# Kernel optimization log

Measured on AMD Instinct MI355X. Metric: run time of the kernel, lower is better.

The kernel has to match this reference:

```python
import jax, jax.numpy as jnp
import numpy as np
from jax import lax

VOCAB, EMB, HID, TAGS = 50000, 300, 512, 50
T, B = 256, 64
H = HID // 2  # per-direction LSTM hidden


def _lstm(xs, W_ih, W_hh, b_ih, b_hh):
    # xs: [T, B, E]; PyTorch gate order i, f, g, o
    xp = jnp.einsum('tbe,ge->tbg', xs, W_ih) + b_ih  # precompute input projection

    def step(carry, x_t):
        h, c = carry
        gates = x_t + h @ W_hh.T + b_hh
        i, f, g, o = jnp.split(gates, 4, axis=-1)
        c = jax.nn.sigmoid(f) * c + jax.nn.sigmoid(i) * jnp.tanh(g)
        h = jax.nn.sigmoid(o) * jnp.tanh(c)
        return (h, c), h

    h0 = jnp.zeros((xs.shape[1], H), xs.dtype)
    _, hs = lax.scan(step, (h0, h0), xp)
    return hs  # [T, B, H]


def setup_inputs() -> dict:
    key = jax.random.key(0)
    ks = jax.random.split(key, 16)
    s_emb = 1.0
    s_lstm = 1.0 / np.sqrt(H)
    inp = {
        'x': jax.random.randint(ks[0], (T, B), 0, VOCAB),
        'y': jax.random.randint(ks[1], (T, B), 0, TAGS),
        'mask': jnp.ones((T, B), dtype=bool),
        'emb': jax.random.normal(ks[2], (VOCAB, EMB), jnp.float32) * s_emb,
        'W_ih_f': jax.random.uniform(ks[3], (4 * H, EMB), jnp.float32, -s_lstm, s_lstm),
        'W_hh_f': jax.random.uniform(ks[4], (4 * H, H), jnp.float32, -s_lstm, s_lstm),
        'b_ih_f': jax.random.uniform(ks[5], (4 * H,), jnp.float32, -s_lstm, s_lstm),
        'b_hh_f': jax.random.uniform(ks[6], (4 * H,), jnp.float32, -s_lstm, s_lstm),
        'W_ih_b': jax.random.uniform(ks[7], (4 * H, EMB), jnp.float32, -s_lstm, s_lstm),
        'W_hh_b': jax.random.uniform(ks[8], (4 * H, H), jnp.float32, -s_lstm, s_lstm),
        'b_ih_b': jax.random.uniform(ks[9], (4 * H,), jnp.float32, -s_lstm, s_lstm),
        'b_hh_b': jax.random.uniform(ks[10], (4 * H,), jnp.float32, -s_lstm, s_lstm),
        'W_out': jax.random.normal(ks[11], (TAGS, HID), jnp.float32) * 0.02,
        'b_out': jnp.zeros((TAGS,), jnp.float32),
        'start_trans': jax.random.uniform(ks[12], (TAGS,), jnp.float32, -0.1, 0.1),
        'end_trans': jax.random.uniform(ks[13], (TAGS,), jnp.float32, -0.1, 0.1),
        'trans': jax.random.uniform(ks[14], (TAGS, TAGS), jnp.float32, -0.1, 0.1),
    }
    return inp


def _emissions(x, emb, W_ih_f, W_hh_f, b_ih_f, b_hh_f, W_ih_b, W_hh_b, b_ih_b, b_hh_b, W_out, b_out):
    e = emb[x]                                   # [T, B, EMB]
    h_f = _lstm(e, W_ih_f, W_hh_f, b_ih_f, b_hh_f)
    h_b = _lstm(e[::-1], W_ih_b, W_hh_b, b_ih_b, b_hh_b)[::-1]
    h = jnp.concatenate([h_f, h_b], axis=-1)    # [T, B, HID]; dropout in eval mode = identity
    return jnp.einsum('tbh,kh->tbk', h, W_out) + b_out  # [T, B, TAGS]


def _crf_loss(em, y, mask, start_trans, end_trans, trans):
    maskf = mask.astype(em.dtype)
    tt = jnp.arange(1, T)
    bb = jnp.arange(B)
    # numerator: score of the gold path (torchcrf _compute_score)
    num = start_trans[y[0]] + em[0, bb, y[0]]
    num = num + (trans[y[:-1], y[1:]] * maskf[1:]).sum(0)
    num = num + (em[tt[:, None], bb[None, :], y[1:]] * maskf[1:]).sum(0)
    last_idx = mask.astype(jnp.int32).sum(0) - 1
    num = num + end_trans[y[last_idx, bb]]
    # denominator: forward algorithm (log-sum-exp DP)
    def fstep(score, inp):
        em_t, m_t = inp
        nxt = jax.nn.logsumexp(score[:, :, None] + trans[None] + em_t[:, None, :], axis=1)
        return jnp.where(m_t[:, None], nxt, score), None
    score0 = start_trans[None] + em[0]          # [B, TAGS]
    score, _ = lax.scan(fstep, score0, (em[1:], mask[1:]))
    denom = jax.nn.logsumexp(score + end_trans[None], axis=-1)
    return -(num - denom).sum()                 # loss = -llh (sum reduction)


def _crf_decode(em, mask, start_trans, end_trans, trans):
    def vstep(score, inp):
        em_t, m_t = inp
        combo = score[:, :, None] + trans[None]  # [B, prev, cur]
        idx = combo.argmax(1)
        nxt = combo.max(1) + em_t
        return jnp.where(m_t[:, None], nxt, score), idx
    score0 = start_trans[None] + em[0]
    score, history = lax.scan(vstep, score0, (em[1:], mask[1:]))  # history: [T-1, B, TAGS]
    last = jnp.argmax(score + end_trans[None], axis=-1)           # [B]
    def bstep(cur, inp):
        hist_t, m_t = inp
        prev = jnp.take_along_axis(hist_t, cur[:, None], axis=1)[:, 0]
        return jnp.where(m_t, prev, cur), cur
    tag0, rest = lax.scan(bstep, last, (history, mask[1:]), reverse=True)
    return jnp.concatenate([tag0[None], rest], axis=0)            # [T, B] int


def reference(x, y, mask, emb, W_ih_f, W_hh_f, b_ih_f, b_hh_f, W_ih_b, W_hh_b, b_ih_b, b_hh_b, W_out, b_out, start_trans, end_trans, trans):
    em = _emissions(x, emb, W_ih_f, W_hh_f, b_ih_f, b_hh_f, W_ih_b, W_hh_b, b_ih_b, b_hh_b, W_out, b_out)
    loss = _crf_loss(em, y, mask, start_trans, end_trans, trans)
    pred = _crf_decode(em, mask, start_trans, end_trans, trans)
    return (loss, pred)
```

## Files before the change

kernel.cpp:

```cpp
#include <hip/hip_runtime.h>
#include <math.h>

#define T_LEN 256
#define BATCH 64
#define NEMB  300
#define NHID  256
#define NG4   1024
#define NTAGS 50

typedef float    f32x4 __attribute__((ext_vector_type(4)));

static constexpr size_t XP_OFF  = 0;
static constexpr size_t XP_SZ   = (size_t)2 * 1024 * 16384;
static constexpr size_t HC_OFF  = XP_OFF + XP_SZ;
static constexpr size_t HC_SZ   = (size_t)T_LEN * 512 * 64;
static constexpr size_t HX_OFF  = HC_OFF + HC_SZ;
static constexpr size_t HX_SZ   = (size_t)2 * 2 * 256 * 64;
static constexpr size_t EM_OFF  = HX_OFF + HX_SZ;
static constexpr size_t EM_SZ   = (size_t)T_LEN * BATCH * NTAGS;
static constexpr size_t LLH_OFF = EM_OFF + EM_SZ;
static constexpr size_t CNT_OFF = LLH_OFF + 64;

__global__ __launch_bounds__(256)
void k_init(float* __restrict__ ws) {
    unsigned int* f = (unsigned int*)(ws + CNT_OFF);
    int i = blockIdx.x * 256 + threadIdx.x;
    if (i < 512) f[i] = 0u;
}

__global__ __launch_bounds__(256)
void k_xp(const int* __restrict__ x, const float* __restrict__ emb,
          const float* __restrict__ Wf, const float* __restrict__ Wb,
          const float* __restrict__ bihf, const float* __restrict__ bhhf,
          const float* __restrict__ bihb, const float* __restrict__ bhhb,
          float* __restrict__ xpT) {
    __shared__ float As[8 * 136];
    __shared__ float Ws[8 * 136];
    __shared__ int   xrow[128];

    const int tid  = threadIdx.x;
    const int row0 = blockIdx.x * 128;
    const int col0 = blockIdx.y * 128;
    const int dir  = col0 >> 10;
    const int g0   = col0 & 1023;
    const float* __restrict__ W   = dir ? Wb   : Wf;
    const float* __restrict__ bih = dir ? bihb : bihf;
    const float* __restrict__ bhh = dir ? bhhb : bhhf;

    if (tid < 128) xrow[tid] = x[row0 + tid];
    __syncthreads();

    float acc[8][8];
#pragma unroll
    for (int i = 0; i < 8; i++)
#pragma unroll
        for (int j = 0; j < 8; j++) acc[i][j] = 0.f;

    const int ty = tid >> 4;
    const int tx = tid & 15;

    for (int kc = 0; kc < NEMB; kc += 8) {
#pragma unroll
        for (int q = 0; q < 4; q++) {
            int idx = tid + 256 * q;
            int r   = idx >> 3;
            int kk  = idx & 7;
            int k   = kc + kk;
            float av = 0.f, wv = 0.f;
            if (k < NEMB) {
                av = emb[(size_t)xrow[r] * NEMB + k];
                wv = W[(size_t)(g0 + r) * NEMB + k];
            }
            As[kk * 136 + r] = av;
            Ws[kk * 136 + r] = wv;
        }
        __syncthreads();
#pragma unroll
        for (int kk = 0; kk < 8; kk++) {
            float4 a0 = *(const float4*)&As[kk * 136 + 8 * ty];
            float4 a1 = *(const float4*)&As[kk * 136 + 8 * ty + 4];
            float4 b0 = *(const float4*)&Ws[kk * 136 + 8 * tx];
            float4 b1 = *(const float4*)&Ws[kk * 136 + 8 * tx + 4];
            float a[8] = {a0.x,a0.y,a0.z,a0.w,a1.x,a1.y,a1.z,a1.w};
            float w[8] = {b0.x,b0.y,b0.z,b0.w,b1.x,b1.y,b1.z,b1.w};
#pragma unroll
            for (int i = 0; i < 8; i++)
#pragma unroll
                for (int j = 0; j < 8; j++) acc[i][j] += a[i] * w[j];
        }
        __syncthreads();
    }

#pragma unroll
    for (int jj = 0; jj < 8; jj++) {
        const int c = g0 + 8 * tx + jj;
        const float bb = bih[c] + bhh[c];
        float4 v0 = make_float4(acc[0][jj] + bb, acc[1][jj] + bb,
                                acc[2][jj] + bb, acc[3][jj] + bb);
        float4 v1 = make_float4(acc[4][jj] + bb, acc[5][jj] + bb,
                                acc[6][jj] + bb, acc[7][jj] + bb);
        float* dst = xpT + ((size_t)dir * 1024 + c) * 16384 + row0 + 8 * ty;
        *(float4*)dst       = v0;
        *(float4*)(dst + 4) = v1;
    }
}

__global__ __launch_bounds__(256, 1)
void k_lstm(const float* __restrict__ xpT, const float* __restrict__ Whf,
            const float* __restrict__ Whb, float* __restrict__ hcatT,
            float* __restrict__ hx, unsigned int* __restrict__ cnt) {
    __shared__ float hs[BATCH * NHID];
    __shared__ float accS[8 * BATCH];

    const int wg    = blockIdx.x;
    const int dir   = wg >> 7;
    const int wslot = wg & 127;
    const int j0    = wslot * 2;
    const int tid   = threadIdx.x;
    const int w     = tid >> 6;
    const int lane  = tid & 63;
    const int rg    = w & 1;
    const int bhalf = w >> 1;
    const int kthr  = lane >> 3;
    const int bthr  = lane & 7;
    const int jme   = j0 + rg;

    const float* __restrict__ Wh  = dir ? Whb : Whf;
    const float* __restrict__ xpd = xpT + (size_t)dir * 1024 * 16384;
    float* __restrict__ hxd = hx + (size_t)dir * 32768;
    unsigned int* __restrict__ cntd = cnt + dir * 256;

    float wreg[4][32];
#pragma unroll
    for (int g = 0; g < 4; ++g) {
        const float4* src = (const float4*)(Wh + ((size_t)(g * 256 + jme)) * 256 + kthr * 32);
#pragma unroll
        for (int q = 0; q < 8; ++q) {
            float4 v = src[q];
            wreg[g][q * 4 + 0] = v.x;
            wreg[g][q * 4 + 1] = v.y;
            wreg[g][q * 4 + 2] = v.z;
            wreg[g][q * 4 + 3] = v.w;
        }
    }
    float creg[2] = {0.f, 0.f};

    for (int s = 0; s < T_LEN; ++s) {
        const int t = dir ? (T_LEN - 1 - s) : s;

        float xq[2][4];
        if (w == 0) {
#pragma unroll
            for (int jj = 0; jj < 2; ++jj)
#pragma unroll
                for (int g = 0; g < 4; ++g)
                    xq[jj][g] = xpd[((size_t)(g * 256 + j0 + jj)) * 16384 + t * 64 + lane];
        }

        float acc[4][4];
#pragma unroll
        for (int g = 0; g < 4; ++g)
#pragma unroll
            for (int bi = 0; bi < 4; ++bi) acc[g][bi] = 0.f;

        if (s > 0) {
            if (tid == 0) {
                while (__hip_atomic_load(&cntd[s - 1], __ATOMIC_RELAXED,
                                         __HIP_MEMORY_SCOPE_AGENT) < 128u) {
                    __builtin_amdgcn_s_sleep(4);
                }
            }
            __syncthreads();

            const float* hsrc = hxd + (size_t)((s - 1) & 1) * 16384;
            f32x4 stv[16];
#pragma unroll
            for (int q = 0; q < 16; ++q) {
                const float* ap = hsrc + q * 1024 + tid * 4;
                asm volatile("global_load_dwordx4 %0, %1, off sc0 sc1"
                             : "=v"(stv[q]) : "v"(ap));
            }
            const int b0   = (tid & 15) * 4;
            const int rot4 = 4 * (tid & 7);
            asm volatile("s_waitcnt vmcnt(8)" ::: "memory");
#pragma unroll
            for (int q = 0; q < 8; ++q) {
                const int kk = q * 16 + (tid >> 4);
                const int sw = (kk & ~31) | ((kk + rot4) & 31);
                hs[(b0 + 0) * 256 + sw] = stv[q].x;
                hs[(b0 + 1) * 256 + sw] = stv[q].y;
                hs[(b0 + 2) * 256 + sw] = stv[q].z;
                hs[(b0 + 3) * 256 + sw] = stv[q].w;
            }
            asm volatile("s_waitcnt vmcnt(0)" ::: "memory");
#pragma unroll
            for (int q = 8; q < 16; ++q) {
                const int kk = q * 16 + (tid >> 4);
                const int sw = (kk & ~31) | ((kk + rot4) & 31);
                hs[(b0 + 0) * 256 + sw] = stv[q].x;
                hs[(b0 + 1) * 256 + sw] = stv[q].y;
                hs[(b0 + 2) * 256 + sw] = stv[q].z;
                hs[(b0 + 3) * 256 + sw] = stv[q].w;
            }
            __syncthreads();

#pragma unroll
            for (int bi = 0; bi < 4; ++bi) {
                const int b = bhalf * 32 + bthr * 4 + bi;
                const float* hb = &hs[b * 256 + kthr * 32];
                const int rot = bthr;
#pragma unroll
                for (int c8 = 0; c8 < 8; ++c8) {
                    const float4 h4 = *(const float4*)&hb[4 * ((c8 + rot) & 7)];
#pragma unroll
                    for (int g = 0; g < 4; ++g) {
                        acc[g][bi] += h4.x * wreg[g][4 * c8 + 0]
                                    + h4.y * wreg[g][4 * c8 + 1]
                                    + h4.z * wreg[g][4 * c8 + 2]
                                    + h4.w * wreg[g][4 * c8 + 3];
                    }
                }
            }
#pragma unroll
            for (int g = 0; g < 4; ++g)
#pragma unroll
                for (int bi = 0; bi < 4; ++bi) {
                    float v = acc[g][bi];
                    v += __shfl_xor(v, 8);
                    v += __shfl_xor(v, 16);
                    v += __shfl_xor(v, 32);
                    acc[g][bi] = v;
                }
            if (kthr == 0) {
#pragma unroll
                for (int g = 0; g < 4; ++g) {
                    float4 v = make_float4(acc[g][0], acc[g][1], acc[g][2], acc[g][3]);
                    *(float4*)&accS[(rg * 4 + g) * 64 + bhalf * 32 + bthr * 4] = v;
                }
            }
            __syncthreads();
        }

        if (w == 0) {
#pragma unroll
            for (int jj = 0; jj < 2; ++jj) {
                float gi = xq[jj][0], gf = xq[jj][1], gg = xq[jj][2], go = xq[jj][3];
                if (s > 0) {
                    gi += accS[(jj * 4 + 0) * 64 + lane];
                    gf += accS[(jj * 4 + 1) * 64 + lane];
                    gg += accS[(jj * 4 + 2) * 64 + lane];
                    go += accS[(jj * 4 + 3) * 64 + lane];
                }
                float ig = 1.f / (1.f + expf(-gi));
                float fg = 1.f / (1.f + expf(-gf));
                float tg = tanhf(gg);
                float og = 1.f / (1.f + expf(-go));
                float cn = fg * creg[jj] + ig * tg;
                creg[jj] = cn;
                float hv = og * tanhf(cn);
                hcatT[(size_t)t * 32768 + (size_t)(dir * 256 + j0 + jj) * 64 + lane] = hv;
                float* hp = &hxd[(size_t)(s & 1) * 16384 + (j0 + jj) * 64 + lane];
                asm volatile("global_store_dword %0, %1, off sc0 sc1"
                             :: "v"(hp), "v"(hv) : "memory");
            }
            if (s < T_LEN - 1) {
                asm volatile("s_waitcnt vmcnt(0)" ::: "memory");
                if (lane == 0) {
                    __hip_atomic_fetch_add(&cntd[s], 1u, __ATOMIC_RELAXED,
                                           __HIP_MEMORY_SCOPE_AGENT);
                }
            }
        }
    }
}

__global__ __launch_bounds__(256)
void k_em(const float* __restrict__ hcatT, const float* __restrict__ Wout,
          const float* __restrict__ bout, float* __restrict__ em) {
    __shared__ float Ws[52 * 132];
    __shared__ float ht[128 * 64];
    const int t   = blockIdx.x;
    const int tid = threadIdx.x;
    const int b   = tid & 63;
    const int tg  = tid >> 6;
    const int tagbase = tg * 13;

    float acc[13];
#pragma unroll
    for (int i = 0; i < 13; i++) acc[i] = 0.f;

    for (int k0 = 0; k0 < 512; k0 += 128) {
        __syncthreads();
#pragma unroll
        for (int q = 0; q < 25; q++) {
            int idx = tid + 256 * q;
            if (idx < 6400) {
                int tag = idx >> 7, kk = idx & 127;
                Ws[tag * 132 + kk] = Wout[(size_t)tag * 512 + k0 + kk];
            }
        }
#pragma unroll
        for (int q = 0; q < 32; q++) {
            int idx = tid + 256 * q;
            ht[idx] = hcatT[(size_t)t * 32768 + (size_t)k0 * 64 + idx];
        }
        __syncthreads();
        for (int kk = 0; kk < 128; kk++) {
            float hv = ht[kk * 64 + b];
#pragma unroll
            for (int i = 0; i < 13; i++)
                acc[i] += hv * Ws[(tagbase + i) * 132 + kk];
        }
    }
#pragma unroll
    for (int i = 0; i < 13; i++) {
        int tag = tagbase + i;
        if (tag < NTAGS)
            em[((size_t)t * BATCH + b) * NTAGS + tag] = acc[i] + bout[tag];
    }
}

__global__ __launch_bounds__(64)
void k_crf_loss(const float* __restrict__ em, const int* __restrict__ y,
                const float* __restrict__ st, const float* __restrict__ et,
                const float* __restrict__ tr, float* __restrict__ llh) {
    __shared__ float trs[2500];
    __shared__ float score[NTAGS];
    __shared__ float red[64];
    const int b   = blockIdx.x;
    const int tid = threadIdx.x;

#pragma unroll
    for (int q = 0; q < 40; q++) {
        int idx = tid + 64 * q;
        if (idx < 2500) trs[idx] = tr[idx];
    }
    __syncthreads();

    float part = 0.f;
    for (int t = tid; t < T_LEN; t += 64) {
        int yt = y[t * BATCH + b];
        if (t == 0) {
            part += st[yt] + em[(size_t)b * NTAGS + yt];
        } else {
            int yp = y[(t - 1) * BATCH + b];
            part += trs[yp * NTAGS + yt] + em[((size_t)t * BATCH + b) * NTAGS + yt];
        }
    }
    red[tid] = part;
    __syncthreads();
    for (int off = 32; off > 0; off >>= 1) {
        if (tid < off) red[tid] += red[tid + off];
        __syncthreads();
    }

    if (tid < NTAGS) score[tid] = st[tid] + em[(size_t)b * NTAGS + tid];
    __syncthreads();

    for (int t = 1; t < T_LEN; t++) {
        float ns = 0.f;
        if (tid < NTAGS) {
            float m = -1e30f;
            for (int p = 0; p < NTAGS; p++) {
                float v = score[p] + trs[p * NTAGS + tid];
                m = fmaxf(m, v);
            }
            float ssum = 0.f;
            for (int p = 0; p < NTAGS; p++) {
                float v = score[p] + trs[p * NTAGS + tid];
                ssum += expf(v - m);
            }
            ns = m + logf(ssum) + em[((size_t)t * BATCH + b) * NTAGS + tid];
        }
        __syncthreads();
        if (tid < NTAGS) score[tid] = ns;
        __syncthreads();
    }

    if (tid == 0) {
        float m = -1e30f;
        for (int cc = 0; cc < NTAGS; cc++) m = fmaxf(m, score[cc] + et[cc]);
        float ssum = 0.f;
        for (int cc = 0; cc < NTAGS; cc++) ssum += expf(score[cc] + et[cc] - m);
        float denom = m + logf(ssum);
        float num = red[0] + et[y[(T_LEN - 1) * BATCH + b]];
        llh[b] = num - denom;
    }
}

__global__ __launch_bounds__(64)
void k_viterbi(const float* __restrict__ em, const float* __restrict__ st,
               const float* __restrict__ et, const float* __restrict__ tr,
               float* __restrict__ out) {
    __shared__ float trs[2500];
    __shared__ float score[NTAGS];
    __shared__ unsigned char hist[(T_LEN - 1) * NTAGS];
    const int b   = blockIdx.x;
    const int tid = threadIdx.x;

#pragma unroll
    for (int q = 0; q < 40; q++) {
        int idx = tid + 64 * q;
        if (idx < 2500) trs[idx] = tr[idx];
    }
    if (tid < NTAGS) score[tid] = st[tid] + em[(size_t)b * NTAGS + tid];
    __syncthreads();

    for (int t = 1; t < T_LEN; t++) {
        float ns = 0.f;
        int am = 0;
        if (tid < NTAGS) {
            float m = -1e30f;
            for (int p = 0; p < NTAGS; p++) {
                float v = score[p] + trs[p * NTAGS + tid];
                if (v > m) { m = v; am = p; }
            }
            ns = m + em[((size_t)t * BATCH + b) * NTAGS + tid];
        }
        __syncthreads();
        if (tid < NTAGS) {
            score[tid] = ns;
            hist[(t - 1) * NTAGS + tid] = (unsigned char)am;
        }
        __syncthreads();
    }

    if (tid == 0) {
        float m = -1e30f;
        int cur = 0;
        for (int cc = 0; cc < NTAGS; cc++) {
            float v = score[cc] + et[cc];
            if (v > m) { m = v; cur = cc; }
        }
        out[1 + (T_LEN - 1) * BATCH + b] = (float)cur;
        for (int t = T_LEN - 2; t >= 0; t--) {
            cur = hist[t * NTAGS + cur];
            out[1 + t * BATCH + b] = (float)cur;
        }
    }
}

__global__ __launch_bounds__(64)
void k_loss_final(const float* __restrict__ llh, float* __restrict__ out) {
    __shared__ float red[64];
    const int tid = threadIdx.x;
    red[tid] = llh[tid];
    __syncthreads();
    for (int off = 32; off > 0; off >>= 1) {
        if (tid < off) red[tid] += red[tid + off];
        __syncthreads();
    }
    if (tid == 0) out[0] = -red[0];
}

extern "C" void kernel_launch(void* const* d_in, const int* in_sizes, int n_in,
                              void* d_out, int out_size, void* d_ws, size_t ws_size,
                              hipStream_t stream) {
    const int*   x    = (const int*)d_in[0];
    const int*   y    = (const int*)d_in[1];
    const float* emb  = (const float*)d_in[3];
    const float* Wihf = (const float*)d_in[4];
    const float* Whhf = (const float*)d_in[5];
    const float* bihf = (const float*)d_in[6];
    const float* bhhf = (const float*)d_in[7];
    const float* Wihb = (const float*)d_in[8];
    const float* Whhb = (const float*)d_in[9];
    const float* bihb = (const float*)d_in[10];
    const float* bhhb = (const float*)d_in[11];
    const float* Wout = (const float*)d_in[12];
    const float* bout = (const float*)d_in[13];
    const float* st   = (const float*)d_in[14];
    const float* et   = (const float*)d_in[15];
    const float* tr   = (const float*)d_in[16];

    float* out  = (float*)d_out;
    float* ws   = (float*)d_ws;
    float* xpT  = ws + XP_OFF;
    float* hcatT= ws + HC_OFF;
    float* hx   = ws + HX_OFF;
    float* em   = ws + EM_OFF;
    float* llh  = ws + LLH_OFF;
    unsigned int* cnt = (unsigned int*)(ws + CNT_OFF);

    hipLaunchKernelGGL(k_init, dim3(2), dim3(256), 0, stream, ws);

    dim3 g1(128, 16);
    hipLaunchKernelGGL(k_xp, g1, dim3(256), 0, stream,
                       x, emb, Wihf, Wihb, bihf, bhhf, bihb, bhhb, xpT);

    hipLaunchKernelGGL(k_lstm, dim3(256), dim3(256), 0, stream,
                       xpT, Whhf, Whhb, hcatT, hx, cnt);

    hipLaunchKernelGGL(k_em, dim3(T_LEN), dim3(256), 0, stream, hcatT, Wout, bout, em);

    hipLaunchKernelGGL(k_crf_loss, dim3(BATCH), dim3(64), 0, stream, em, y, st, et, tr, llh);

    hipLaunchKernelGGL(k_viterbi, dim3(BATCH), dim3(64), 0, stream, em, st, et, tr, out);

    hipLaunchKernelGGL(k_loss_final, dim3(1), dim3(64), 0, stream, llh, out);
}
```

Before: 3.475 ms.

## Shard LSTM step barrier counters across cache lines and stagger h loads

Replaces the single per-step arrival counter with eight counters, one per group of 16 workgroups, each padded onto its own 64-byte stride. A full wavefront now polls all eight with a ballot and a shorter sleep, which is meant to cut atomic contention and shorten barrier latency on the grid-wide recurrence. Each workgroup also rotates the order of its hidden-state loads by its slot index, to spread simultaneous reads across memory channels. The launch adds about 30 KB of dynamic shared memory, apparently to force one workgroup per CU. In exchange, the init kernel has to clear a much larger counter array, and every wait does more polling traffic.

Result: slower. 4.330 ms (+24.6%).

```diff
diff --git a/kernel.cpp b/kernel.cpp
--- a/kernel.cpp
+++ b/kernel.cpp
@@ -20,12 +20,13 @@
 static constexpr size_t EM_SZ   = (size_t)T_LEN * BATCH * NTAGS;
 static constexpr size_t LLH_OFF = EM_OFF + EM_SZ;
 static constexpr size_t CNT_OFF = LLH_OFF + 64;
+static constexpr int    CNT_DWORDS = 2 * 256 * 128;
 
 __global__ __launch_bounds__(256)
 void k_init(float* __restrict__ ws) {
     unsigned int* f = (unsigned int*)(ws + CNT_OFF);
     int i = blockIdx.x * 256 + threadIdx.x;
-    if (i < 512) f[i] = 0u;
+    if (i < CNT_DWORDS) f[i] = 0u;
 }
 
 __global__ __launch_bounds__(256)
@@ -111,6 +112,7 @@
             float* __restrict__ hx, unsigned int* __restrict__ cnt) {
     __shared__ float hs[BATCH * NHID];
     __shared__ float accS[8 * BATCH];
+    extern __shared__ float dynpad[];
 
     const int wg    = blockIdx.x;
     const int dir   = wg >> 7;
@@ -125,10 +127,13 @@
     const int bthr  = lane & 7;
     const int jme   = j0 + rg;
 
+    dynpad[tid] = 0.f;
+
     const float* __restrict__ Wh  = dir ? Whb : Whf;
     const float* __restrict__ xpd = xpT + (size_t)dir * 1024 * 16384;
     float* __restrict__ hxd = hx + (size_t)dir * 32768;
-    unsigned int* __restrict__ cntd = cnt + dir * 256;
+    unsigned int* __restrict__ cntd = cnt + (size_t)dir * 256 * 128;
+    const int grp = wslot >> 4;
 
     float wreg[4][32];
 #pragma unroll
@@ -164,19 +169,25 @@
             for (int bi = 0; bi < 4; ++bi) acc[g][bi] = 0.f;
 
         if (s > 0) {
-            if (tid == 0) {
-                while (__hip_atomic_load(&cntd[s - 1], __ATOMIC_RELAXED,
-                                         __HIP_MEMORY_SCOPE_AGENT) < 128u) {
-                    __builtin_amdgcn_s_sleep(4);
+            if (w == 1) {
+                const unsigned int* cp = cntd + (size_t)(s - 1) * 128 + (lane & 7) * 16;
+                while (true) {
+                    unsigned v = __hip_atomic_load(cp, __ATOMIC_RELAXED,
+                                                   __HIP_MEMORY_SCOPE_AGENT);
+                    if (__ballot(v >= 16u) == ~0ull) break;
+                    __builtin_amdgcn_s_sleep(1);
                 }
             }
             __syncthreads();
 
             const float* hsrc = hxd + (size_t)((s - 1) & 1) * 16384;
             f32x4 stv[16];
+            int   kks[16];
 #pragma unroll
             for (int q = 0; q < 16; ++q) {
-                const float* ap = hsrc + q * 1024 + tid * 4;
+                const int qq = (q + wslot) & 15;
+                kks[q] = qq * 16 + (tid >> 4);
+                const float* ap = hsrc + qq * 1024 + tid * 4;
                 asm volatile("global_load_dwordx4 %0, %1, off sc0 sc1"
                              : "=v"(stv[q]) : "v"(ap));
             }
@@ -185,7 +196,7 @@
             asm volatile("s_waitcnt vmcnt(8)" ::: "memory");
 #pragma unroll
             for (int q = 0; q < 8; ++q) {
-                const int kk = q * 16 + (tid >> 4);
+                const int kk = kks[q];
                 const int sw = (kk & ~31) | ((kk + rot4) & 31);
                 hs[(b0 + 0) * 256 + sw] = stv[q].x;
                 hs[(b0 + 1) * 256 + sw] = stv[q].y;
@@ -195,7 +206,7 @@
             asm volatile("s_waitcnt vmcnt(0)" ::: "memory");
 #pragma unroll
             for (int q = 8; q < 16; ++q) {
-                const int kk = q * 16 + (tid >> 4);
+                const int kk = kks[q];
                 const int sw = (kk & ~31) | ((kk + rot4) & 31);
                 hs[(b0 + 0) * 256 + sw] = stv[q].x;
                 hs[(b0 + 1) * 256 + sw] = stv[q].y;
@@ -266,8 +277,8 @@
             if (s < T_LEN - 1) {
                 asm volatile("s_waitcnt vmcnt(0)" ::: "memory");
                 if (lane == 0) {
-                    __hip_atomic_fetch_add(&cntd[s], 1u, __ATOMIC_RELAXED,
-                                           __HIP_MEMORY_SCOPE_AGENT);
+                    __hip_atomic_fetch_add(&cntd[(size_t)s * 128 + grp * 16], 1u,
+                                           __ATOMIC_RELAXED, __HIP_MEMORY_SCOPE_AGENT);
                 }
             }
         }
@@ -482,13 +493,13 @@
     float* llh  = ws + LLH_OFF;
     unsigned int* cnt = (unsigned int*)(ws + CNT_OFF);
 
-    hipLaunchKernelGGL(k_init, dim3(2), dim3(256), 0, stream, ws);
+    hipLaunchKernelGGL(k_init, dim3(256), dim3(256), 0, stream, ws);
 
     dim3 g1(128, 16);
     hipLaunchKernelGGL(k_xp, g1, dim3(256), 0, stream,
                        x, emb, Wihf, Wihb, bihf, bhhf, bihb, bhhb, xpT);
 
-    hipLaunchKernelGGL(k_lstm, dim3(256), dim3(256), 0, stream,
+    hipLaunchKernelGGL(k_lstm, dim3(256), dim3(256), 30 * 1024, stream,
                        xpT, Whhf, Whhb, hcatT, hx, cnt);
 
     hipLaunchKernelGGL(k_em, dim3(T_LEN), dim3(256), 0, stream, hcatT, Wout, bout, em);
```
